# Optimization experiments

Hardware: AMD Instinct MI355X
Metric: run time of the kernel (lower is better)

## Reference

```python
import jax, jax.numpy as jnp
import numpy as np
from jax import lax

V_VOX, T_PTS, D, H, W = 12000, 35, 10, 200, 176
EPS = 1e-5


def _bn(x, g, b, axes, shape):
    m = x.mean(axes, keepdims=True)
    v = x.var(axes, keepdims=True)  # biased var, matches torch BN training stats
    return g.reshape(shape) * (x - m) * lax.rsqrt(v + EPS) + b.reshape(shape)


def _conv3d(x, w, b):
    y = lax.conv_general_dilated(x, w, (1, 1, 1), 'SAME',
                                 dimension_numbers=('NCDHW', 'OIDHW', 'NCDHW'))
    return y + b[None, :, None, None, None]


def _conv2d(x, w, b):
    y = lax.conv_general_dilated(x, w, (1, 1), 'SAME',
                                 dimension_numbers=('NCHW', 'OIHW', 'NCHW'))
    return y + b[None, :, None, None]


def setup_inputs() -> dict:
    key = jax.random.key(0)
    ks = jax.random.split(key, 12)
    voxels = jax.random.normal(ks[0], (1, V_VOX, T_PTS, 4), jnp.float32)
    # unique voxel coordinates (the torch loop overwrites on duplicates; unique avoids ambiguity)
    rng = np.random.default_rng(0)
    flat = rng.choice(D * H * W, size=V_VOX, replace=False)
    z = flat // (H * W); rem = flat % (H * W)
    coords = jnp.asarray(np.stack([z, rem // W, rem % W], axis=1), dtype=jnp.int32)
    s = 0.05
    p = dict(
        w_lin=jax.random.normal(ks[1], (32, 4), jnp.float32) * s,
        b_lin=jnp.zeros((32,), jnp.float32),
        g_bn0=jnp.ones((32,), jnp.float32), be_bn0=jnp.zeros((32,), jnp.float32),
        w_c3a=jax.random.normal(ks[2], (64, 32, 3, 3, 3), jnp.float32) * s,
        b_c3a=jnp.zeros((64,), jnp.float32),
        g_bn1=jnp.ones((64,), jnp.float32), be_bn1=jnp.zeros((64,), jnp.float32),
        w_c3b=jax.random.normal(ks[3], (64, 64, 3, 3, 3), jnp.float32) * s,
        b_c3b=jnp.zeros((64,), jnp.float32),
        g_bn2=jnp.ones((64,), jnp.float32), be_bn2=jnp.zeros((64,), jnp.float32),
        w_r1=jax.random.normal(ks[4], (128, 64, 3, 3), jnp.float32) * s,
        b_r1=jnp.zeros((128,), jnp.float32),
        w_r2=jax.random.normal(ks[5], (8, 128, 1, 1), jnp.float32) * s,
        b_r2=jnp.zeros((8,), jnp.float32),
    )
    return dict(voxels=voxels, coords=coords, **p)


def reference(voxels, coords, w_lin, b_lin, g_bn0, be_bn0,
              w_c3a, b_c3a, g_bn1, be_bn1, w_c3b, b_c3b, g_bn2, be_bn2,
              w_r1, b_r1, w_r2, b_r2):
    B, V, T, C = voxels.shape
    # SimpleVFE: linear -> BN1d (batch stats) -> relu -> max over points
    h = voxels.reshape(B * V * T, C) @ w_lin.T + b_lin          # [BVT,32]
    h = jax.nn.relu(_bn(h, g_bn0, be_bn0, 0, (1, 32)))
    feats = h.reshape(B, V, T, 32).max(axis=2)                  # [B,V,32]
    # fused scatter into dense volume (replaces per-voxel python loop)
    volume = jnp.zeros((B, 32, D, H, W), voxels.dtype)
    volume = volume.at[0, :, coords[:, 0], coords[:, 1], coords[:, 2]].set(feats[0])
    # 3D backbone
    x = jax.nn.relu(_bn(_conv3d(volume, w_c3a, b_c3a), g_bn1, be_bn1, (0, 2, 3, 4), (1, 64, 1, 1, 1)))
    x = jax.nn.relu(_bn(_conv3d(x, w_c3b, b_c3b), g_bn2, be_bn2, (0, 2, 3, 4), (1, 64, 1, 1, 1)))
    x = x.mean(axis=2)                                          # collapse depth -> [B,64,H,W]
    # RPN head
    out = _conv2d(jax.nn.relu(_conv2d(x, w_r1, b_r1)), w_r2, b_r2)  # [B,8,H,W]
    box = jnp.concatenate([out[:, 0:3], jnp.exp(out[:, 3:6]),
                           jnp.tanh(out[:, 6:7]), jax.nn.sigmoid(out[:, 7:8])], axis=1)
    return box
```

## Files before the change

kernel.cpp:

```cpp
#include <hip/hip_runtime.h>
#include <math.h>

#define V_VOX 12000
#define T_PTS 35
#define DD 10
#define HH 200
#define WW 176
#define EPSV 1e-5f

#define DP 12
#define HP 202
#define WP 178
#define PPLN (HP * WP)
#define PVOX (DP * PPLN)
#define NPIX (DD * HH * WW)
#define HWPIX (HH * WW)

typedef _Float16 half_t;
typedef _Float16 f16x8 __attribute__((ext_vector_type(8)));
typedef float f32x4 __attribute__((ext_vector_type(4)));

#define WPA_OFF 0
#define WPB_OFF 110592
#define WPR1_OFF 331776
#define STATS_OFF 479232
#define FEATS_OFF 483328
#define VOLP_OFF 2019328
#define X1P_OFF 29633536
#define Y_OFF 84861952
#define PLANE_OFF 129917952
#define R1OUT_OFF 134520320

#define S_BN0S 0
#define S_BN0Q 32
#define S_BN1S 64
#define S_BN1Q 128
#define S_BN2S 192
#define S_BN2Q 256
#define C0A 320
#define C0B 352
#define C1A 384
#define C1B 448
#define C2A 512
#define C2B 576

__global__ void k_pack(const float* __restrict__ w, half_t* __restrict__ wp,
                       int IC, int NT, int OC) {
    int id = blockIdx.x * 256 + threadIdx.x;
    int OCT = OC >> 4, KH = IC >> 5;
    int total = NT * KH * OCT * 512;
    if (id >= total) return;
    int j = id & 7;
    int lane = (id >> 3) & 63;
    int rest = id >> 9;
    int ot = rest % OCT; rest /= OCT;
    int kh = rest % KH;
    int tap = rest / KH;
    int oc = ot * 16 + (lane & 15);
    int ic = kh * 32 + (lane >> 4) * 8 + j;
    wp[id] = (half_t)w[(oc * IC + ic) * NT + tap];
}

__global__ void k_vfe_stats(const float4* __restrict__ vox, const float* __restrict__ w_lin,
                            const float* __restrict__ b_lin, float* __restrict__ S) {
    int tid = blockIdx.x * 256 + threadIdx.x;
    int c = threadIdx.x & 31;
    float4 w = ((const float4*)w_lin)[c];
    float bl = b_lin[c];
    float s = 0.f, q = 0.f;
    const int np = V_VOX * T_PTS;
    int stride = gridDim.x * 8;
    for (int p = tid >> 5; p < np; p += stride) {
        float4 v = vox[p];
        float d = v.x * w.x + v.y * w.y + v.z * w.z + v.w * w.w + bl;
        s += d;
        q += d * d;
    }
    s += __shfl_xor(s, 32);
    q += __shfl_xor(q, 32);
    if ((threadIdx.x & 63) < 32) {
        atomicAdd(&S[S_BN0S + c], s);
        atomicAdd(&S[S_BN0Q + c], q);
    }
}

__global__ void k_bn_final(const float* __restrict__ ss, const float* __restrict__ sq,
                           const float* __restrict__ g, const float* __restrict__ be,
                           float* __restrict__ ca, float* __restrict__ cb, int C, float invN) {
    int c = threadIdx.x;
    if (c >= C) return;
    float m = ss[c] * invN;
    float v = sq[c] * invN - m * m;
    float a = g[c] * rsqrtf(v + EPSV);
    ca[c] = a;
    cb[c] = be[c] - m * a;
}

__global__ void k_vfe_max(const float4* __restrict__ vox, const float* __restrict__ w_lin,
                          const float* __restrict__ b_lin, const float* __restrict__ ca,
                          const float* __restrict__ cb, float* __restrict__ feats) {
    int id = blockIdx.x * 256 + threadIdx.x;
    if (id >= V_VOX * 32) return;
    int c = id & 31;
    int v = id >> 5;
    float4 w = ((const float4*)w_lin)[c];
    float bl = b_lin[c], A = ca[c], B = cb[c];
    float m = 0.f;
    for (int t = 0; t < T_PTS; t++) {
        float4 p = vox[v * T_PTS + t];
        float d = p.x * w.x + p.y * w.y + p.z * w.z + p.w * w.w + bl;
        m = fmaxf(m, A * d + B);
    }
    feats[id] = m;
}

__global__ void k_scatter(const float* __restrict__ feats, const int* __restrict__ coords,
                          half_t* __restrict__ volp) {
    int id = blockIdx.x * 256 + threadIdx.x;
    if (id >= V_VOX * 32) return;
    int c = id & 31;
    int v = id >> 5;
    int z = coords[v * 3 + 0];
    int y = coords[v * 3 + 1];
    int x = coords[v * 3 + 2];
    volp[(((z + 1) * HP + (y + 1)) * WP + (x + 1)) * 32 + c] = (half_t)feats[id];
}

template <int KH, int CLDS, int DZ, int OCTP, bool RELU, bool STATS>
__global__ __launch_bounds__(256, 4) void k_conv(const half_t* __restrict__ in,
                                                 const half_t* __restrict__ wp,
                                                 const float* __restrict__ bias,
                                                 half_t* __restrict__ out,
                                                 float* __restrict__ ssum,
                                                 float* __restrict__ ssq) {
    constexpr int CIN = KH * 32;
    constexpr int C8 = KH * 4;
    constexpr int TOT8 = 18 * 18 * C8;
    constexpr int OC = OCTP * 16;
    __shared__ half_t tile[18 * 18 * CLDS];

    const int tid = threadIdx.x;
    const int lane = tid & 63;
    const int wv = tid >> 6;
    const int x0 = blockIdx.x * 16;
    const int y0b = blockIdx.y * 16;
    const int z0 = (DZ == 3) ? blockIdx.z : 0;
    const int ocb = (DZ == 3) ? 0 : blockIdx.z * 4;
    const int y0w = y0b + wv * 4;
    const bool valid = (y0w < HH);
    const int colc = lane & 15, grp = lane >> 4;

    f32x4 acc[4][4];
#pragma unroll
    for (int m = 0; m < 4; m++)
#pragma unroll
        for (int n = 0; n < 4; n++) acc[m][n] = (f32x4)(0.f);

#pragma unroll 1
    for (int dz = 0; dz < DZ; ++dz) {
        const half_t* sl = in + (size_t)(z0 + dz) * (DZ == 3 ? (size_t)HP * WP * CIN : 0);
#pragma unroll
        for (int it = 0; it < (TOT8 + 255) / 256; ++it) {
            int e = it * 256 + tid;
            if (e < TOT8) {
                int ch8 = e % C8;
                int pxr = e / C8;
                int px = pxr % 18;
                int row = pxr / 18;
                int srow = y0b + row;
                if (srow > HP - 1) srow = HP - 1;
                const half_t* s = sl + ((size_t)srow * WP + x0 + px) * CIN + ch8 * 8;
                *(f16x8*)&tile[pxr * CLDS + ch8 * 8] = *(const f16x8*)s;
            }
        }
        __syncthreads();

        if (valid) {
#pragma unroll 1
            for (int dx = 0; dx < 3; ++dx) {
#pragma unroll
                for (int kh = 0; kh < KH; ++kh) {
                    f16x8 Af[6];
#pragma unroll
                    for (int r = 0; r < 6; ++r)
                        Af[r] = *(const f16x8*)&tile[((wv * 4 + r) * 18 + colc + dx) * CLDS
                                                     + kh * 32 + grp * 8];
                    f16x8 Bf[3][4];
#pragma unroll
                    for (int dy = 0; dy < 3; ++dy) {
                        const half_t* wb = wp + ((size_t)((dz * 9 + dy * 3 + dx) * KH + kh) * OCTP
                                                 + ocb) * 512 + lane * 8;
#pragma unroll
                        for (int n = 0; n < 4; ++n) Bf[dy][n] = *(const f16x8*)(wb + n * 512);
                    }
#pragma unroll
                    for (int dy = 0; dy < 3; ++dy)
#pragma unroll
                        for (int m = 0; m < 4; ++m)
#pragma unroll
                            for (int n = 0; n < 4; ++n)
                                acc[m][n] = __builtin_amdgcn_mfma_f32_16x16x32_f16(
                                    Af[dy + m], Bf[dy][n], acc[m][n], 0, 0, 0);
                }
            }
        }
        __syncthreads();
    }

    if (!valid) return;
#pragma unroll
    for (int n = 0; n < 4; ++n) {
        int oc = (ocb + n) * 16 + colc;
        float bv = bias[oc];
        float s = 0.f, q = 0.f;
#pragma unroll
        for (int m = 0; m < 4; ++m) {
            int yy = y0w + m;
#pragma unroll
            for (int i = 0; i < 4; ++i) {
                int xx = x0 + grp * 4 + i;
                float v = acc[m][n][i] + bv;
                if (STATS) { s += v; q += v * v; }
                float w = RELU ? fmaxf(v, 0.f) : v;
                out[((size_t)(z0 * HH + yy) * WW + xx) * OC + oc] = (half_t)w;
            }
        }
        if (STATS) {
            s += __shfl_xor(s, 16); s += __shfl_xor(s, 32);
            q += __shfl_xor(q, 16); q += __shfl_xor(q, 32);
            if (lane < 16) {
                atomicAdd(&ssum[oc], s);
                atomicAdd(&ssq[oc], q);
            }
        }
    }
}

__global__ void k_activate(const half_t* __restrict__ y1, const float* __restrict__ ca,
                           const float* __restrict__ cb, half_t* __restrict__ xp) {
    int id = blockIdx.x * 256 + threadIdx.x;
    if (id >= PVOX * 8) return;
    int c0 = (id & 7) * 8;
    int pix = id >> 3;
    int zp = pix / PPLN;
    int rem = pix - zp * PPLN;
    int yp = rem / WP;
    int xq = rem - yp * WP;
    f16x8 o;
    if (zp >= 1 && zp <= DD && yp >= 1 && yp <= HH && xq >= 1 && xq <= WW) {
        size_t p = ((size_t)((zp - 1) * HH + (yp - 1)) * WW + (xq - 1));
        f16x8 v = *(const f16x8*)(y1 + p * 64 + c0);
#pragma unroll
        for (int j = 0; j < 8; j++)
            o[j] = (half_t)fmaxf(ca[c0 + j] * (float)v[j] + cb[c0 + j], 0.f);
    } else {
#pragma unroll
        for (int j = 0; j < 8; j++) o[j] = (half_t)0.f;
    }
    *(f16x8*)(xp + (size_t)pix * 64 + c0) = o;
}

__global__ void k_depthmean(const half_t* __restrict__ y2, const float* __restrict__ ca,
                            const float* __restrict__ cb, half_t* __restrict__ plane) {
    int id = blockIdx.x * 256 + threadIdx.x;
    int c = id & 63;
    int pix = id >> 6;
    int yp = pix / WP;
    int xq = pix - yp * WP;
    float val = 0.f;
    if (yp >= 1 && yp <= HH && xq >= 1 && xq <= WW) {
        float A = ca[c], B = cb[c], s = 0.f;
        const half_t* base = y2 + ((size_t)(yp - 1) * WW + (xq - 1)) * 64 + c;
#pragma unroll
        for (int z = 0; z < DD; z++)
            s += fmaxf(A * (float)base[(size_t)z * HWPIX * 64] + B, 0.f);
        val = s * 0.1f;
    }
    plane[(size_t)pix * 64 + c] = (half_t)val;
}

__global__ void k_r2(const half_t* __restrict__ r1o, const float* __restrict__ w,
                     const float* __restrict__ bias, float* __restrict__ outp) {
    __shared__ float wsm[1024];
    for (int i = threadIdx.x; i < 1024; i += 256) wsm[i] = w[i];
    __syncthreads();
    int p = blockIdx.x * 256 + threadIdx.x;
    if (p >= HWPIX) return;
    float acc[8];
#pragma unroll
    for (int o = 0; o < 8; o++) acc[o] = bias[o];
    const half_t* rb = r1o + (size_t)p * 128;
#pragma unroll 4
    for (int icb = 0; icb < 128; icb += 8) {
        f16x8 v = *(const f16x8*)(rb + icb);
#pragma unroll
        for (int j = 0; j < 8; j++) {
            float vv = (float)v[j];
#pragma unroll
            for (int o = 0; o < 8; o++) acc[o] += vv * wsm[o * 128 + icb + j];
        }
    }
    outp[0 * HWPIX + p] = acc[0];
    outp[1 * HWPIX + p] = acc[1];
    outp[2 * HWPIX + p] = acc[2];
    outp[3 * HWPIX + p] = expf(acc[3]);
    outp[4 * HWPIX + p] = expf(acc[4]);
    outp[5 * HWPIX + p] = expf(acc[5]);
    outp[6 * HWPIX + p] = tanhf(acc[6]);
    outp[7 * HWPIX + p] = 1.f / (1.f + expf(-acc[7]));
}

extern "C" void kernel_launch(void* const* d_in, const int* in_sizes, int n_in,
                              void* d_out, int out_size, void* d_ws, size_t ws_size,
                              hipStream_t stream) {
    const float4* voxels = (const float4*)d_in[0];
    const int* coords = (const int*)d_in[1];
    const float* w_lin = (const float*)d_in[2];
    const float* b_lin = (const float*)d_in[3];
    const float* g_bn0 = (const float*)d_in[4];
    const float* be_bn0 = (const float*)d_in[5];
    const float* w_c3a = (const float*)d_in[6];
    const float* b_c3a = (const float*)d_in[7];
    const float* g_bn1 = (const float*)d_in[8];
    const float* be_bn1 = (const float*)d_in[9];
    const float* w_c3b = (const float*)d_in[10];
    const float* b_c3b = (const float*)d_in[11];
    const float* g_bn2 = (const float*)d_in[12];
    const float* be_bn2 = (const float*)d_in[13];
    const float* w_r1 = (const float*)d_in[14];
    const float* b_r1 = (const float*)d_in[15];
    const float* w_r2 = (const float*)d_in[16];
    const float* b_r2 = (const float*)d_in[17];

    char* ws = (char*)d_ws;
    half_t* wpA = (half_t*)(ws + WPA_OFF);
    half_t* wpB = (half_t*)(ws + WPB_OFF);
    half_t* wpR1 = (half_t*)(ws + WPR1_OFF);
    float* S = (float*)(ws + STATS_OFF);
    float* feats = (float*)(ws + FEATS_OFF);
    half_t* volp = (half_t*)(ws + VOLP_OFF);
    half_t* x1p = (half_t*)(ws + X1P_OFF);
    half_t* Y = (half_t*)(ws + Y_OFF);
    half_t* plane = (half_t*)(ws + PLANE_OFF);
    half_t* r1out = (half_t*)(ws + R1OUT_OFF);
    float* outp = (float*)d_out;

    hipMemsetAsync(S, 0, 320 * sizeof(float), stream);
    hipMemsetAsync(volp, 0, (size_t)PVOX * 32 * sizeof(half_t), stream);

    k_pack<<<216, 256, 0, stream>>>(w_c3a, wpA, 32, 27, 64);
    k_pack<<<432, 256, 0, stream>>>(w_c3b, wpB, 64, 27, 64);
    k_pack<<<288, 256, 0, stream>>>(w_r1, wpR1, 64, 9, 128);

    k_vfe_stats<<<512, 256, 0, stream>>>(voxels, w_lin, b_lin, S);
    k_bn_final<<<1, 64, 0, stream>>>(S + S_BN0S, S + S_BN0Q, g_bn0, be_bn0,
                                     S + C0A, S + C0B, 32, 1.f / 420000.f);
    k_vfe_max<<<1500, 256, 0, stream>>>(voxels, w_lin, b_lin, S + C0A, S + C0B, feats);
    k_scatter<<<1500, 256, 0, stream>>>(feats, coords, volp);

    k_conv<1, 40, 3, 4, false, true><<<dim3(11, 13, 10), 256, 0, stream>>>(
        volp, wpA, b_c3a, Y, S + S_BN1S, S + S_BN1Q);
    k_bn_final<<<1, 64, 0, stream>>>(S + S_BN1S, S + S_BN1Q, g_bn1, be_bn1,
                                     S + C1A, S + C1B, 64, 1.f / 352000.f);
    k_activate<<<13484, 256, 0, stream>>>(Y, S + C1A, S + C1B, x1p);

    k_conv<2, 72, 3, 4, false, true><<<dim3(11, 13, 10), 256, 0, stream>>>(
        x1p, wpB, b_c3b, Y, S + S_BN2S, S + S_BN2Q);
    k_bn_final<<<1, 64, 0, stream>>>(S + S_BN2S, S + S_BN2Q, g_bn2, be_bn2,
                                     S + C2A, S + C2B, 64, 1.f / 352000.f);

    k_depthmean<<<8989, 256, 0, stream>>>(Y, S + C2A, S + C2B, plane);

    k_conv<2, 72, 1, 8, true, false><<<dim3(11, 13, 2), 256, 0, stream>>>(
        plane, wpR1, b_r1, r1out, nullptr, nullptr);
    k_r2<<<138, 256, 0, stream>>>(r1out, w_r2, b_r2, outp);
}
```

Before: 512.4 us.

## Split conv input channels into 32-channel planes to shrink LDS tile and raise occupancy

The padded activation and plane buffers now store channels as separate 32-channel planes instead of interleaved 64 channels. The conv kernel loads and consumes one 32-channel slab at a time into a fixed 40-stride LDS tile, and launch bounds rise from 4 to 5 blocks per CU. This roughly halves shared memory per block for the 64-channel convs, which should allow more resident blocks. The cost is an extra sync and tile reload per channel half, and the per-kh loop no longer overlaps the two halves' loads with MFMA work.

Measured after the change: 819.5 us. +59.9%, slower.

```diff
diff --git a/kernel.cpp b/kernel.cpp
--- a/kernel.cpp
+++ b/kernel.cpp
@@ -43,6 +43,8 @@
 #define C1B 448
 #define C2A 512
 #define C2B 576
+
+#define CLDS 40
 
 __global__ void k_pack(const float* __restrict__ w, half_t* __restrict__ wp,
                        int IC, int NT, int OC) {
@@ -126,17 +128,16 @@
     volp[(((z + 1) * HP + (y + 1)) * WP + (x + 1)) * 32 + c] = (half_t)feats[id];
 }
 
-template <int KH, int CLDS, int DZ, int OCTP, bool RELU, bool STATS>
-__global__ __launch_bounds__(256, 4) void k_conv(const half_t* __restrict__ in,
+template <int KH, int DZ, int OCTP, bool RELU, bool STATS>
+__global__ __launch_bounds__(256, 5) void k_conv(const half_t* __restrict__ in,
+                                                 size_t khstride,
                                                  const half_t* __restrict__ wp,
                                                  const float* __restrict__ bias,
                                                  half_t* __restrict__ out,
                                                  float* __restrict__ ssum,
                                                  float* __restrict__ ssq) {
-    constexpr int CIN = KH * 32;
-    constexpr int C8 = KH * 4;
-    constexpr int TOT8 = 18 * 18 * C8;
     constexpr int OC = OCTP * 16;
+    constexpr int TOT8 = 18 * 18 * 4;
     __shared__ half_t tile[18 * 18 * CLDS];
 
     const int tid = threadIdx.x;
@@ -158,33 +159,34 @@
 
 #pragma unroll 1
     for (int dz = 0; dz < DZ; ++dz) {
-        const half_t* sl = in + (size_t)(z0 + dz) * (DZ == 3 ? (size_t)HP * WP * CIN : 0);
-#pragma unroll
-        for (int it = 0; it < (TOT8 + 255) / 256; ++it) {
-            int e = it * 256 + tid;
-            if (e < TOT8) {
-                int ch8 = e % C8;
-                int pxr = e / C8;
-                int px = pxr % 18;
-                int row = pxr / 18;
-                int srow = y0b + row;
-                if (srow > HP - 1) srow = HP - 1;
-                const half_t* s = sl + ((size_t)srow * WP + x0 + px) * CIN + ch8 * 8;
-                *(f16x8*)&tile[pxr * CLDS + ch8 * 8] = *(const f16x8*)s;
+#pragma unroll 1
+        for (int kh = 0; kh < KH; ++kh) {
+            const half_t* sl = in + (size_t)kh * khstride
+                               + (size_t)(z0 + dz) * (DZ == 3 ? (size_t)PPLN * 32 : 0);
+#pragma unroll
+            for (int it = 0; it < 6; ++it) {
+                int e = it * 256 + tid;
+                if (e < TOT8) {
+                    int ch8 = e & 3;
+                    int pxr = e >> 2;
+                    int px = pxr % 18;
+                    int row = pxr / 18;
+                    int srow = y0b + row;
+                    if (srow > HP - 1) srow = HP - 1;
+                    const half_t* s = sl + ((size_t)srow * WP + x0 + px) * 32 + ch8 * 8;
+                    *(f16x8*)&tile[pxr * CLDS + ch8 * 8] = *(const f16x8*)s;
+                }
             }
-        }
-        __syncthreads();
-
-        if (valid) {
-#pragma unroll 1
-            for (int dx = 0; dx < 3; ++dx) {
-#pragma unroll
-                for (int kh = 0; kh < KH; ++kh) {
+            __syncthreads();
+
+            if (valid) {
+#pragma unroll
+                for (int dx = 0; dx < 3; ++dx) {
                     f16x8 Af[6];
 #pragma unroll
                     for (int r = 0; r < 6; ++r)
                         Af[r] = *(const f16x8*)&tile[((wv * 4 + r) * 18 + colc + dx) * CLDS
-                                                     + kh * 32 + grp * 8];
+                                                     + grp * 8];
                     f16x8 Bf[3][4];
 #pragma unroll
                     for (int dy = 0; dy < 3; ++dy) {
@@ -203,8 +205,8 @@
                                     Af[dy + m], Bf[dy][n], acc[m][n], 0, 0, 0);
                 }
             }
+            __syncthreads();
         }
-        __syncthreads();
     }
 
     if (!valid) return;
@@ -257,7 +259,8 @@
 #pragma unroll
         for (int j = 0; j < 8; j++) o[j] = (half_t)0.f;
     }
-    *(f16x8*)(xp + (size_t)pix * 64 + c0) = o;
+    int khp = c0 >> 5;
+    *(f16x8*)(xp + (size_t)khp * PVOX * 32 + (size_t)pix * 32 + (c0 & 31)) = o;
 }
 
 __global__ void k_depthmean(const half_t* __restrict__ y2, const float* __restrict__ ca,
@@ -276,7 +279,8 @@
             s += fmaxf(A * (float)base[(size_t)z * HWPIX * 64] + B, 0.f);
         val = s * 0.1f;
     }
-    plane[(size_t)pix * 64 + c] = (half_t)val;
+    int khp = c >> 5;
+    plane[(size_t)khp * PPLN * 32 + (size_t)pix * 32 + (c & 31)] = (half_t)val;
 }
 
 __global__ void k_r2(const half_t* __restrict__ r1o, const float* __restrict__ w,
@@ -358,20 +362,20 @@
     k_vfe_max<<<1500, 256, 0, stream>>>(voxels, w_lin, b_lin, S + C0A, S + C0B, feats);
     k_scatter<<<1500, 256, 0, stream>>>(feats, coords, volp);
 
-    k_conv<1, 40, 3, 4, false, true><<<dim3(11, 13, 10), 256, 0, stream>>>(
-        volp, wpA, b_c3a, Y, S + S_BN1S, S + S_BN1Q);
+    k_conv<1, 3, 4, false, true><<<dim3(11, 13, 10), 256, 0, stream>>>(
+        volp, 0, wpA, b_c3a, Y, S + S_BN1S, S + S_BN1Q);
     k_bn_final<<<1, 64, 0, stream>>>(S + S_BN1S, S + S_BN1Q, g_bn1, be_bn1,
                                      S + C1A, S + C1B, 64, 1.f / 352000.f);
     k_activate<<<13484, 256, 0, stream>>>(Y, S + C1A, S + C1B, x1p);
 
-    k_conv<2, 72, 3, 4, false, true><<<dim3(11, 13, 10), 256, 0, stream>>>(
-        x1p, wpB, b_c3b, Y, S + S_BN2S, S + S_BN2Q);
+    k_conv<2, 3, 4, false, true><<<dim3(11, 13, 10), 256, 0, stream>>>(
+        x1p, (size_t)PVOX * 32, wpB, b_c3b, Y, S + S_BN2S, S + S_BN2Q);
     k_bn_final<<<1, 64, 0, stream>>>(S + S_BN2S, S + S_BN2Q, g_bn2, be_bn2,
                                      S + C2A, S + C2B, 64, 1.f / 352000.f);
 
     k_depthmean<<<8989, 256, 0, stream>>>(Y, S + C2A, S + C2B, plane);
 
-    k_conv<2, 72, 1, 8, true, false><<<dim3(11, 13, 2), 256, 0, stream>>>(
-        plane, wpR1, b_r1, r1out, nullptr, nullptr);
+    k_conv<2, 1, 8, true, false><<<dim3(11, 13, 2), 256, 0, stream>>>(
+        plane, (size_t)PPLN * 32, wpR1, b_r1, r1out, nullptr, nullptr);
     k_r2<<<138, 256, 0, stream>>>(r1out, w_r2, b_r2, outp);
 }
```
